# Kernel optimization log

Measured on AMD Instinct MI355X. Metric: run time of the kernel, lower is better.

The kernel has to match this reference:

```python
import jax, jax.numpy as jnp
import numpy as np

BN_EPS = 1e-5
Q_EPS = 1e-8

def quant_weight(w):
    # per-output-channel median-abs scale, ternary quantization
    s = jnp.median(jnp.abs(w).reshape(w.shape[0], -1), axis=1)
    s = jnp.maximum(s, Q_EPS)[:, None, None, None]
    return jnp.clip(jnp.round(w / s), -1.0, 1.0) * s

def bitconv(x, w, b, stride, pad):
    wq = quant_weight(w)
    y = jax.lax.conv_general_dilated(
        x, wq, (stride, stride), [(pad, pad), (pad, pad)],
        dimension_numbers=('NCHW', 'OIHW', 'NCHW'))
    return y + b[None, :, None, None]

def bn(x, g, b, m, v):
    scale = g / jnp.sqrt(v + BN_EPS)
    return x * scale[None, :, None, None] + (b - m * scale)[None, :, None, None]

def setup_inputs() -> dict:
    key = jax.random.key(0)
    ks = jax.random.split(key, 20)
    B, Cin, H, W = 64, 1024, 14, 14
    width, Cout = 256, 1024  # planes=256, expansion=4
    d = {}
    d['x'] = jax.random.normal(ks[0], (B, Cin, H, W), jnp.float32)
    d['w1'] = jax.random.normal(ks[1], (width, Cin, 1, 1), jnp.float32) * 0.05
    d['b1'] = jax.random.normal(ks[2], (width,), jnp.float32) * 0.01
    d['g1'] = jax.random.uniform(ks[3], (width,), jnp.float32, 0.5, 1.5)
    d['be1'] = jax.random.normal(ks[4], (width,), jnp.float32) * 0.1
    d['m1'] = jax.random.normal(ks[5], (width,), jnp.float32) * 0.1
    d['v1'] = jax.random.uniform(ks[6], (width,), jnp.float32, 0.5, 1.5)
    d['w2'] = jax.random.normal(ks[7], (width, width, 3, 3), jnp.float32) * 0.05
    d['b2'] = jax.random.normal(ks[8], (width,), jnp.float32) * 0.01
    d['g2'] = jax.random.uniform(ks[9], (width,), jnp.float32, 0.5, 1.5)
    d['be2'] = jax.random.normal(ks[10], (width,), jnp.float32) * 0.1
    d['m2'] = jax.random.normal(ks[11], (width,), jnp.float32) * 0.1
    d['v2'] = jax.random.uniform(ks[12], (width,), jnp.float32, 0.5, 1.5)
    d['w3'] = jax.random.normal(ks[13], (Cout, width, 1, 1), jnp.float32) * 0.05
    d['b3'] = jax.random.normal(ks[14], (Cout,), jnp.float32) * 0.01
    d['g3'] = jax.random.uniform(ks[15], (Cout,), jnp.float32, 0.5, 1.5)
    d['be3'] = jax.random.normal(ks[16], (Cout,), jnp.float32) * 0.1
    d['m3'] = jax.random.normal(ks[17], (Cout,), jnp.float32) * 0.1
    d['v3'] = jax.random.uniform(ks[18], (Cout,), jnp.float32, 0.5, 1.5)
    return d

def reference(x, w1, b1, g1, be1, m1, v1,
              w2, b2, g2, be2, m2, v2,
              w3, b3, g3, be3, m3, v3):
    out = jax.nn.silu(bn(bitconv(x, w1, b1, 1, 0), g1, be1, m1, v1))
    out = jax.nn.silu(bn(bitconv(out, w2, b2, 1, 1), g2, be2, m2, v2))
    out = bn(bitconv(out, w3, b3, 1, 0), g3, be3, m3, v3)
    return jax.nn.silu(out + x)
```

## Files before the change

### kernel.cpp

```cpp
#include <hip/hip_runtime.h>
#include <cstdint>
#include <cstddef>

typedef unsigned short u16;
typedef unsigned int u32;
typedef __attribute__((ext_vector_type(4))) float f32x4;
typedef __attribute__((ext_vector_type(8))) short s16x8;

__device__ __forceinline__ u16 f2bf(float f) {
  u32 u = __float_as_uint(f);
  u = (u + 0x7fffu + ((u >> 16) & 1u)) >> 16;
  return (u16)u;
}

__device__ __forceinline__ float silu_f(float y) {
  return y / (1.0f + __expf(-y));
}

template<int N, int REMAP>
__global__ __launch_bounds__(256) void quant_kernel(
    const float* __restrict__ w, const float* __restrict__ bias,
    const float* __restrict__ g, const float* __restrict__ be,
    const float* __restrict__ mu, const float* __restrict__ var,
    u16* __restrict__ wq, float* __restrict__ alpha, float* __restrict__ beta)
{
  constexpr int NV = N / 64;
  __shared__ int hist[4 * 256];

  const int tid = threadIdx.x;
  const int wave = tid >> 6;
  const int lane = tid & 63;
  const int ch = blockIdx.x * 4 + wave;
  const int wb = wave * 256;

  u32 vals[NV];
  const float* wp = w + (size_t)ch * N;
  #pragma unroll
  for (int t = 0; t < NV; ++t)
    vals[t] = __float_as_uint(wp[lane + 64 * t]);

  const int r0 = N / 2;
  int r = r0;
  u32 prefix = 0;
  #pragma unroll
  for (int pass = 0; pass < 4; ++pass) {
    const int shift = 24 - 8 * pass;
    hist[wb + lane] = 0;
    hist[wb + 64 + lane] = 0;
    hist[wb + 128 + lane] = 0;
    hist[wb + 192 + lane] = 0;
    __syncthreads();
    #pragma unroll
    for (int t = 0; t < NV; ++t) {
      u32 a = vals[t] & 0x7fffffffu;
      bool cand;
      if (pass == 0) cand = true;
      else cand = ((a >> (shift + 8)) == (prefix >> (shift + 8)));
      if (cand) atomicAdd(&hist[wb + ((a >> shift) & 255)], 1);
    }
    __syncthreads();
    int h0 = hist[wb + 4 * lane + 0];
    int h1 = hist[wb + 4 * lane + 1];
    int h2 = hist[wb + 4 * lane + 2];
    int h3 = hist[wb + 4 * lane + 3];
    int s4 = h0 + h1 + h2 + h3;
    int cum = s4;
    #pragma unroll
    for (int off = 1; off < 64; off <<= 1) {
      int tt = __shfl_up(cum, off);
      if (lane >= off) cum += tt;
    }
    int pre = cum - s4;
    bool sel = (r > pre) && (r <= cum);
    unsigned long long bal = __ballot(sel);
    int src = __ffsll((unsigned long long)bal) - 1;
    int c0 = pre + h0, c1 = c0 + h1, c2 = c1 + h2;
    int d_l, nr_l;
    if (r <= c0)      { d_l = 4 * lane + 0; nr_l = r - pre; }
    else if (r <= c1) { d_l = 4 * lane + 1; nr_l = r - c0; }
    else if (r <= c2) { d_l = 4 * lane + 2; nr_l = r - c1; }
    else              { d_l = 4 * lane + 3; nr_l = r - c2; }
    int d = __shfl(d_l, src);
    r = __shfl(nr_l, src);
    prefix |= (u32)d << shift;
    __syncthreads();
  }
  const u32 v0 = prefix;

  int cle = 0;
  u32 mn = 0xFFFFFFFFu;
  #pragma unroll
  for (int t = 0; t < NV; ++t) {
    u32 a = vals[t] & 0x7fffffffu;
    cle += (a <= v0) ? 1 : 0;
    if (a > v0) mn = min(mn, a);
  }
  #pragma unroll
  for (int off = 1; off < 64; off <<= 1) {
    cle += __shfl_xor(cle, off);
    mn = min(mn, (u32)__shfl_xor((int)mn, off));
  }
  u32 v1 = (cle >= r0 + 1) ? v0 : mn;

  float s = 0.5f * (__uint_as_float(v0) + __uint_as_float(v1));
  s = fmaxf(s, 1e-8f);

  #pragma unroll
  for (int t = 0; t < NV; ++t) {
    int i = lane + 64 * t;
    float q = rintf(__uint_as_float(vals[t]) / s);
    q = fminf(fmaxf(q, -1.0f), 1.0f);
    int oi;
    if (REMAP) {
      int cin = i / 9, tap = i - cin * 9;
      oi = tap * 256 + cin;
    } else {
      oi = i;
    }
    wq[(size_t)ch * N + oi] = f2bf(q);
  }
  if (lane == 0) {
    float sc = g[ch] / sqrtf(var[ch] + 1e-5f);
    alpha[ch] = s * sc;
    beta[ch] = (bias[ch] - mu[ch]) * sc + be[ch];
  }
}

__global__ __launch_bounds__(256) void transpose_cast_kernel(
    const float* __restrict__ x, u16* __restrict__ xb)
{
  __shared__ u16 tile[64 * 198];
  const int n = blockIdx.x;
  const int c0 = blockIdx.y * 64;
  const float* xp = x + ((size_t)n * 1024 + c0) * 196;
  for (int i = threadIdx.x; i < 64 * 196; i += 256) {
    int c = i / 196, hw = i - c * 196;
    tile[c * 198 + hw] = f2bf(xp[i]);
  }
  __syncthreads();
  u16* op = xb + (size_t)n * 196 * 1024 + c0;
  for (int i = threadIdx.x; i < 64 * 196; i += 256) {
    int hw = i >> 6, c = i & 63;
    op[(size_t)hw * 1024 + c] = tile[c * 198 + hw];
  }
}

template<int MODE, int KTOT>
__global__ __launch_bounds__(256, 2) void gemm_kernel(
    const u16* __restrict__ Wq, const u16* __restrict__ Bact,
    const float* __restrict__ alpha, const float* __restrict__ beta,
    u16* __restrict__ outb, float* __restrict__ outf, const float* __restrict__ xres)
{
  constexpr int BK = 64;
  constexpr int NKT = KTOT / BK;
  __shared__ u16 As[128 * BK];
  __shared__ u16 Bs[128 * BK];
  __shared__ int rowbase[128];
  __shared__ float aS[128], bS[128];

  const int tid = threadIdx.x;
  const int jb = blockIdx.x * 128;
  const int cb = blockIdx.y * 128;
  const int wave = tid >> 6;
  const int lane = tid & 63;
  const int wm = (wave & 1) * 64;
  const int wn = (wave >> 1) * 64;
  const int quad = lane >> 4;
  const int l16 = lane & 15;

  if (tid < 128) {
    aS[tid] = alpha[cb + tid];
    bS[tid] = beta[cb + tid];
    if (MODE == 2) {
      int j = jb + tid;
      int n = j / 196, hw = j - n * 196;
      int h = hw / 14, w = hw - h * 14;
      rowbase[tid] = ((n * 16 + h) * 16 + w) * 256;
    }
  }
  __syncthreads();

  f32x4 acc[4][4];
  #pragma unroll
  for (int a = 0; a < 4; ++a)
    #pragma unroll
    for (int b = 0; b < 4; ++b)
      acc[a][b] = {0.f, 0.f, 0.f, 0.f};

  const int row_s = tid >> 3;
  const int cc_s = tid & 7;

  for (int kt = 0; kt < NKT; ++kt) {
    {
      const uint4* gp = reinterpret_cast<const uint4*>(Wq + (size_t)cb * KTOT + kt * BK);
      #pragma unroll
      for (int i = 0; i < 4; ++i) {
        int row = row_s + 32 * i;
        uint4 v = gp[(size_t)row * (KTOT / 8) + cc_s];
        *reinterpret_cast<uint4*>(&As[row * BK + ((cc_s ^ (row & 7)) << 3)]) = v;
      }
    }
    if (MODE == 2) {
      int tap = kt >> 2;
      int c0 = (kt & 3) * 64;
      int dy = tap / 3, dx = tap - dy * 3;
      int tapoff = (dy * 16 + dx) * 256 + c0;
      const uint4* gp = reinterpret_cast<const uint4*>(Bact);
      #pragma unroll
      for (int i = 0; i < 4; ++i) {
        int row = row_s + 32 * i;
        uint4 v = gp[((rowbase[row] + tapoff) >> 3) + cc_s];
        *reinterpret_cast<uint4*>(&Bs[row * BK + ((cc_s ^ (row & 7)) << 3)]) = v;
      }
    } else {
      const uint4* gp = reinterpret_cast<const uint4*>(Bact + (size_t)jb * KTOT + kt * BK);
      #pragma unroll
      for (int i = 0; i < 4; ++i) {
        int row = row_s + 32 * i;
        uint4 v = gp[(size_t)row * (KTOT / 8) + cc_s];
        *reinterpret_cast<uint4*>(&Bs[row * BK + ((cc_s ^ (row & 7)) << 3)]) = v;
      }
    }
    __syncthreads();

    #pragma unroll
    for (int s = 0; s < 2; ++s) {
      s16x8 af[4], bf[4];
      #pragma unroll
      for (int mi = 0; mi < 4; ++mi) {
        int row = wm + mi * 16 + l16;
        int kc = s * 4 + quad;
        af[mi] = *reinterpret_cast<const s16x8*>(&As[row * BK + ((kc ^ (row & 7)) << 3)]);
      }
      #pragma unroll
      for (int ni = 0; ni < 4; ++ni) {
        int row = wn + ni * 16 + l16;
        int kc = s * 4 + quad;
        bf[ni] = *reinterpret_cast<const s16x8*>(&Bs[row * BK + ((kc ^ (row & 7)) << 3)]);
      }
      #pragma unroll
      for (int mi = 0; mi < 4; ++mi)
        #pragma unroll
        for (int ni = 0; ni < 4; ++ni)
          acc[mi][ni] = __builtin_amdgcn_mfma_f32_16x16x32_bf16(af[mi], bf[ni], acc[mi][ni], 0, 0, 0);
    }
    __syncthreads();
  }

  #pragma unroll
  for (int mi = 0; mi < 4; ++mi) {
    const int lc = wm + mi * 16 + quad * 4;
    #pragma unroll
    for (int ni = 0; ni < 4; ++ni) {
      const int j = jb + wn + ni * 16 + l16;
      if (MODE == 1) {
        int n = j / 196, hw = j - n * 196;
        int h = hw / 14, w = hw - h * 14;
        size_t base = (size_t)(((n * 16 + h + 1) * 16) + (w + 1)) * 256 + cb + lc;
        ushort4 pk;
        float y;
        y = silu_f(aS[lc + 0] * acc[mi][ni][0] + bS[lc + 0]); pk.x = f2bf(y);
        y = silu_f(aS[lc + 1] * acc[mi][ni][1] + bS[lc + 1]); pk.y = f2bf(y);
        y = silu_f(aS[lc + 2] * acc[mi][ni][2] + bS[lc + 2]); pk.z = f2bf(y);
        y = silu_f(aS[lc + 3] * acc[mi][ni][3] + bS[lc + 3]); pk.w = f2bf(y);
        *reinterpret_cast<ushort4*>(&outb[base]) = pk;
      } else if (MODE == 2) {
        size_t base = (size_t)j * 256 + cb + lc;
        ushort4 pk;
        float y;
        y = silu_f(aS[lc + 0] * acc[mi][ni][0] + bS[lc + 0]); pk.x = f2bf(y);
        y = silu_f(aS[lc + 1] * acc[mi][ni][1] + bS[lc + 1]); pk.y = f2bf(y);
        y = silu_f(aS[lc + 2] * acc[mi][ni][2] + bS[lc + 2]); pk.z = f2bf(y);
        y = silu_f(aS[lc + 3] * acc[mi][ni][3] + bS[lc + 3]); pk.w = f2bf(y);
        *reinterpret_cast<ushort4*>(&outb[base]) = pk;
      } else {
        int n = j / 196, hw = j - n * 196;
        #pragma unroll
        for (int r = 0; r < 4; ++r) {
          int c = cb + lc + r;
          size_t idx = (size_t)n * 200704 + (size_t)c * 196 + hw;
          float y = aS[lc + r] * acc[mi][ni][r] + bS[lc + r] + xres[idx];
          outf[idx] = silu_f(y);
        }
      }
    }
  }
}

extern "C" void kernel_launch(void* const* d_in, const int* in_sizes, int n_in,
                              void* d_out, int out_size, void* d_ws, size_t ws_size,
                              hipStream_t stream)
{
  const float* x   = (const float*)d_in[0];
  const float* w1  = (const float*)d_in[1];
  const float* b1  = (const float*)d_in[2];
  const float* g1  = (const float*)d_in[3];
  const float* be1 = (const float*)d_in[4];
  const float* m1  = (const float*)d_in[5];
  const float* v1  = (const float*)d_in[6];
  const float* w2  = (const float*)d_in[7];
  const float* b2  = (const float*)d_in[8];
  const float* g2  = (const float*)d_in[9];
  const float* be2 = (const float*)d_in[10];
  const float* m2  = (const float*)d_in[11];
  const float* v2  = (const float*)d_in[12];
  const float* w3  = (const float*)d_in[13];
  const float* b3  = (const float*)d_in[14];
  const float* g3  = (const float*)d_in[15];
  const float* be3 = (const float*)d_in[16];
  const float* m3  = (const float*)d_in[17];
  const float* v3  = (const float*)d_in[18];
  float* out = (float*)d_out;

  uint8_t* ws = (uint8_t*)d_ws;
  u16* xb    = (u16*)(ws);
  u16* act1p = (u16*)(ws + 25690112ull);
  u16* act2  = (u16*)(ws + 34078720ull);
  u16* w1q   = (u16*)(ws + 40501248ull);
  u16* w2q   = (u16*)(ws + 41025536ull);
  u16* w3q   = (u16*)(ws + 42205184ull);
  float* a1c = (float*)(ws + 42729472ull);
  float* b1c = a1c + 256;
  float* a2c = b1c + 256;
  float* b2c = a2c + 256;
  float* a3c = b2c + 256;
  float* b3c = a3c + 1024;

  hipMemsetAsync(act1p, 0, 8388608ull, stream);

  transpose_cast_kernel<<<dim3(64, 16), 256, 0, stream>>>(x, xb);
  quant_kernel<1024, 0><<<64, 256, 0, stream>>>(w1, b1, g1, be1, m1, v1, w1q, a1c, b1c);
  quant_kernel<2304, 1><<<64, 256, 0, stream>>>(w2, b2, g2, be2, m2, v2, w2q, a2c, b2c);
  quant_kernel<256, 0><<<256, 256, 0, stream>>>(w3, b3, g3, be3, m3, v3, w3q, a3c, b3c);

  gemm_kernel<1, 1024><<<dim3(98, 2), 256, 0, stream>>>(w1q, xb, a1c, b1c, act1p, (float*)nullptr, (const float*)nullptr);
  gemm_kernel<2, 2304><<<dim3(98, 2), 256, 0, stream>>>(w2q, act1p, a2c, b2c, act2, (float*)nullptr, (const float*)nullptr);
  gemm_kernel<3, 256><<<dim3(98, 8), 256, 0, stream>>>(w3q, act2, a3c, b3c, (u16*)nullptr, out, x);
}
```

Baseline: 279.8 us.

## Halve GEMM N-tile for first two convs and stage final epilogue through LDS

Adds a BJ template parameter so the 1x1 and 3x3 GEMMs use 64-wide spatial tiles, doubling the grid from 196 to 392 blocks so more of the GPU's compute units get work. The final GEMM's residual+SiLU epilogue now stages scaled accumulators in shared memory and writes NCHW output with coalesced float4 loads and stores, instead of strided scalar accesses. The smaller tiles reduce per-block data reuse, and the epilogue adds extra barriers and LDS traffic.

```diff
diff --git a/kernel.cpp b/kernel.cpp
--- a/kernel.cpp
+++ b/kernel.cpp
@@ -145,7 +145,7 @@
   }
 }
 
-template<int MODE, int KTOT>
+template<int MODE, int KTOT, int BJ>
 __global__ __launch_bounds__(256, 2) void gemm_kernel(
     const u16* __restrict__ Wq, const u16* __restrict__ Bact,
     const float* __restrict__ alpha, const float* __restrict__ beta,
@@ -153,38 +153,44 @@
 {
   constexpr int BK = 64;
   constexpr int NKT = KTOT / BK;
-  __shared__ u16 As[128 * BK];
-  __shared__ u16 Bs[128 * BK];
-  __shared__ int rowbase[128];
-  __shared__ float aS[128], bS[128];
+  constexpr int NI = BJ / 32;
+  constexpr int SMEM_SIZE = (MODE == 3) ? 34816 : (16384 + BJ * BK * 2 + BJ * 4 + 1024);
+
+  __shared__ __align__(16) char smem[SMEM_SIZE];
+  u16* As = (u16*)smem;
+  u16* Bs = (u16*)(smem + 16384);
+  int* rowbase = (int*)(smem + 16384 + BJ * BK * 2);
+  float* aS = (float*)(MODE == 3 ? (smem + 33792) : (smem + 16384 + BJ * BK * 2 + BJ * 4));
+  float* bS = aS + 128;
+  float* lbuf = (float*)smem;
 
   const int tid = threadIdx.x;
-  const int jb = blockIdx.x * 128;
+  const int jb = blockIdx.x * BJ;
   const int cb = blockIdx.y * 128;
   const int wave = tid >> 6;
   const int lane = tid & 63;
   const int wm = (wave & 1) * 64;
-  const int wn = (wave >> 1) * 64;
+  const int wn = (wave >> 1) * (BJ / 2);
   const int quad = lane >> 4;
   const int l16 = lane & 15;
 
   if (tid < 128) {
     aS[tid] = alpha[cb + tid];
     bS[tid] = beta[cb + tid];
-    if (MODE == 2) {
-      int j = jb + tid;
-      int n = j / 196, hw = j - n * 196;
-      int h = hw / 14, w = hw - h * 14;
-      rowbase[tid] = ((n * 16 + h) * 16 + w) * 256;
-    }
+  }
+  if (MODE == 2 && tid < BJ) {
+    int j = jb + tid;
+    int n = j / 196, hw = j - n * 196;
+    int h = hw / 14, w = hw - h * 14;
+    rowbase[tid] = ((n * 16 + h) * 16 + w) * 256;
   }
   __syncthreads();
 
-  f32x4 acc[4][4];
+  f32x4 acc[4][NI];
   #pragma unroll
   for (int a = 0; a < 4; ++a)
     #pragma unroll
-    for (int b = 0; b < 4; ++b)
+    for (int b = 0; b < NI; ++b)
       acc[a][b] = {0.f, 0.f, 0.f, 0.f};
 
   const int row_s = tid >> 3;
@@ -207,7 +213,7 @@
       int tapoff = (dy * 16 + dx) * 256 + c0;
       const uint4* gp = reinterpret_cast<const uint4*>(Bact);
       #pragma unroll
-      for (int i = 0; i < 4; ++i) {
+      for (int i = 0; i < BJ / 32; ++i) {
         int row = row_s + 32 * i;
         uint4 v = gp[((rowbase[row] + tapoff) >> 3) + cc_s];
         *reinterpret_cast<uint4*>(&Bs[row * BK + ((cc_s ^ (row & 7)) << 3)]) = v;
@@ -215,7 +221,7 @@
     } else {
       const uint4* gp = reinterpret_cast<const uint4*>(Bact + (size_t)jb * KTOT + kt * BK);
       #pragma unroll
-      for (int i = 0; i < 4; ++i) {
+      for (int i = 0; i < BJ / 32; ++i) {
         int row = row_s + 32 * i;
         uint4 v = gp[(size_t)row * (KTOT / 8) + cc_s];
         *reinterpret_cast<uint4*>(&Bs[row * BK + ((cc_s ^ (row & 7)) << 3)]) = v;
@@ -225,7 +231,7 @@
 
     #pragma unroll
     for (int s = 0; s < 2; ++s) {
-      s16x8 af[4], bf[4];
+      s16x8 af[4], bf[NI];
       #pragma unroll
       for (int mi = 0; mi < 4; ++mi) {
         int row = wm + mi * 16 + l16;
@@ -233,7 +239,7 @@
         af[mi] = *reinterpret_cast<const s16x8*>(&As[row * BK + ((kc ^ (row & 7)) << 3)]);
       }
       #pragma unroll
-      for (int ni = 0; ni < 4; ++ni) {
+      for (int ni = 0; ni < NI; ++ni) {
         int row = wn + ni * 16 + l16;
         int kc = s * 4 + quad;
         bf[ni] = *reinterpret_cast<const s16x8*>(&Bs[row * BK + ((kc ^ (row & 7)) << 3)]);
@@ -241,48 +247,73 @@
       #pragma unroll
       for (int mi = 0; mi < 4; ++mi)
         #pragma unroll
-        for (int ni = 0; ni < 4; ++ni)
+        for (int ni = 0; ni < NI; ++ni)
           acc[mi][ni] = __builtin_amdgcn_mfma_f32_16x16x32_bf16(af[mi], bf[ni], acc[mi][ni], 0, 0, 0);
     }
     __syncthreads();
   }
 
-  #pragma unroll
-  for (int mi = 0; mi < 4; ++mi) {
-    const int lc = wm + mi * 16 + quad * 4;
-    #pragma unroll
-    for (int ni = 0; ni < 4; ++ni) {
-      const int j = jb + wn + ni * 16 + l16;
-      if (MODE == 1) {
-        int n = j / 196, hw = j - n * 196;
-        int h = hw / 14, w = hw - h * 14;
-        size_t base = (size_t)(((n * 16 + h + 1) * 16) + (w + 1)) * 256 + cb + lc;
+  if (MODE == 1 || MODE == 2) {
+    #pragma unroll
+    for (int mi = 0; mi < 4; ++mi) {
+      const int lc = wm + mi * 16 + quad * 4;
+      #pragma unroll
+      for (int ni = 0; ni < NI; ++ni) {
+        const int j = jb + wn + ni * 16 + l16;
         ushort4 pk;
         float y;
         y = silu_f(aS[lc + 0] * acc[mi][ni][0] + bS[lc + 0]); pk.x = f2bf(y);
         y = silu_f(aS[lc + 1] * acc[mi][ni][1] + bS[lc + 1]); pk.y = f2bf(y);
         y = silu_f(aS[lc + 2] * acc[mi][ni][2] + bS[lc + 2]); pk.z = f2bf(y);
         y = silu_f(aS[lc + 3] * acc[mi][ni][3] + bS[lc + 3]); pk.w = f2bf(y);
+        size_t base;
+        if (MODE == 1) {
+          int n = j / 196, hw = j - n * 196;
+          int h = hw / 14, w = hw - h * 14;
+          base = (size_t)(((n * 16 + h + 1) * 16) + (w + 1)) * 256 + cb + lc;
+        } else {
+          base = (size_t)j * 256 + cb + lc;
+        }
         *reinterpret_cast<ushort4*>(&outb[base]) = pk;
-      } else if (MODE == 2) {
-        size_t base = (size_t)j * 256 + cb + lc;
-        ushort4 pk;
-        float y;
-        y = silu_f(aS[lc + 0] * acc[mi][ni][0] + bS[lc + 0]); pk.x = f2bf(y);
-        y = silu_f(aS[lc + 1] * acc[mi][ni][1] + bS[lc + 1]); pk.y = f2bf(y);
-        y = silu_f(aS[lc + 2] * acc[mi][ni][2] + bS[lc + 2]); pk.z = f2bf(y);
-        y = silu_f(aS[lc + 3] * acc[mi][ni][3] + bS[lc + 3]); pk.w = f2bf(y);
-        *reinterpret_cast<ushort4*>(&outb[base]) = pk;
-      } else {
-        int n = j / 196, hw = j - n * 196;
+      }
+    }
+  } else {
+    #pragma unroll
+    for (int k = 0; k < 2; ++k) {
+      if ((wave & 1) == k) {
         #pragma unroll
-        for (int r = 0; r < 4; ++r) {
-          int c = cb + lc + r;
-          size_t idx = (size_t)n * 200704 + (size_t)c * 196 + hw;
-          float y = aS[lc + r] * acc[mi][ni][r] + bS[lc + r] + xres[idx];
-          outf[idx] = silu_f(y);
+        for (int mi = 0; mi < 4; ++mi) {
+          const int cl = mi * 16 + quad * 4;
+          const int gc = 64 * k + cl;
+          #pragma unroll
+          for (int ni = 0; ni < 4; ++ni) {
+            const int jj = wn + ni * 16 + l16;
+            #pragma unroll
+            for (int r = 0; r < 4; ++r)
+              lbuf[(cl + r) * 132 + jj] = aS[gc + r] * acc[mi][ni][r] + bS[gc + r];
+          }
         }
       }
+      __syncthreads();
+      #pragma unroll
+      for (int it = 0; it < 8; ++it) {
+        int idx = tid + it * 256;
+        int cl = idx >> 5;
+        int jg = idx & 31;
+        int c = cb + 64 * k + cl;
+        int j0 = jb + jg * 4;
+        int n = j0 / 196, hw = j0 - n * 196;
+        size_t o = (size_t)n * 200704 + (size_t)c * 196 + hw;
+        float4 lv = *reinterpret_cast<float4*>(&lbuf[cl * 132 + jg * 4]);
+        float4 xv = *reinterpret_cast<const float4*>(&xres[o]);
+        float4 ov;
+        ov.x = silu_f(lv.x + xv.x);
+        ov.y = silu_f(lv.y + xv.y);
+        ov.z = silu_f(lv.z + xv.z);
+        ov.w = silu_f(lv.w + xv.w);
+        *reinterpret_cast<float4*>(&outf[o]) = ov;
+      }
+      __syncthreads();
     }
   }
 }
@@ -333,7 +364,7 @@
   quant_kernel<2304, 1><<<64, 256, 0, stream>>>(w2, b2, g2, be2, m2, v2, w2q, a2c, b2c);
   quant_kernel<256, 0><<<256, 256, 0, stream>>>(w3, b3, g3, be3, m3, v3, w3q, a3c, b3c);
 
-  gemm_kernel<1, 1024><<<dim3(98, 2), 256, 0, stream>>>(w1q, xb, a1c, b1c, act1p, (float*)nullptr, (const float*)nullptr);
-  gemm_kernel<2, 2304><<<dim3(98, 2), 256, 0, stream>>>(w2q, act1p, a2c, b2c, act2, (float*)nullptr, (const float*)nullptr);
-  gemm_kernel<3, 256><<<dim3(98, 8), 256, 0, stream>>>(w3q, act2, a3c, b3c, (u16*)nullptr, out, x);
-}
+  gemm_kernel<1, 1024, 64><<<dim3(196, 2), 256, 0, stream>>>(w1q, xb, a1c, b1c, act1p, (float*)nullptr, (const float*)nullptr);
+  gemm_kernel<2, 2304, 64><<<dim3(196, 2), 256, 0, stream>>>(w2q, act1p, a2c, b2c, act2, (float*)nullptr, (const float*)nullptr);
+  gemm_kernel<3, 256, 128><<<dim3(98, 8), 256, 0, stream>>>(w3q, act2, a3c, b3c, (u16*)nullptr, out, x);
+}
```

Measured after the change: 282.1 us. No clear change (+0.8%).
